# Kernel optimization log

Hardware: AMD Instinct MI355X
Metric: run time of the kernel (lower is better)

Reference implementation:

```python
import jax, jax.numpy as jnp
import numpy as np

N = 50000
E = 1600000
NFEAT = 256
NHID = 256
PAD_N = 60000


def setup_inputs() -> dict:
    key = jax.random.key(0)
    ks = jax.random.split(key, 8)
    x = jax.random.normal(ks[0], (N, NFEAT), dtype=jnp.float32)
    adj_rows = jax.random.randint(ks[1], (E,), 0, N)
    adj_cols = jax.random.randint(ks[2], (E,), 0, N)
    adj_vals = jax.random.uniform(ks[3], (E,), dtype=jnp.float32)
    pos_idx = jnp.arange(N)  # unique rows within padded output
    W1 = jax.random.normal(ks[4], (NFEAT, NHID), dtype=jnp.float32) * 0.05
    b1 = jax.random.normal(ks[5], (NHID,), dtype=jnp.float32) * 0.05
    W2 = jax.random.normal(ks[6], (NHID, NHID), dtype=jnp.float32) * 0.05
    b2 = jax.random.normal(ks[7], (NHID,), dtype=jnp.float32) * 0.05
    return {"x": x, "adj_rows": adj_rows, "adj_cols": adj_cols,
            "adj_vals": adj_vals, "pad_n": PAD_N, "pos_idx": pos_idx,
            "W1": W1, "b1": b1, "W2": W2, "b2": b2}


def _graph_conv(x, rows, cols, vals, W, b):
    # support = x @ W ; out = adj @ support + b  (adj in COO form)
    support = x @ W                                   # [N, H]
    msgs = vals[:, None] * support[cols]              # [E, H] gather + scale
    agg = jax.ops.segment_sum(msgs, rows, num_segments=x.shape[0])
    return agg + b


def reference(x, adj_rows, adj_cols, adj_vals, pad_n, pos_idx, W1, b1, W2, b2):
    h = jax.nn.relu(_graph_conv(x, adj_rows, adj_cols, adj_vals, W1, b1))
    # dropout: eval mode (training=False) -> identity
    h = jax.nn.relu(_graph_conv(h, adj_rows, adj_cols, adj_vals, W2, b2))
    out = jnp.zeros((pad_n, h.shape[1]), dtype=h.dtype)
    out = out.at[pos_idx].set(h)
    return out
```

## Files before the change

kernel.cpp:

```cpp
#include <hip/hip_runtime.h>
#include <hip/hip_bf16.h>

typedef __attribute__((ext_vector_type(8))) short short8;
typedef __attribute__((ext_vector_type(4))) float f32x4;
typedef __attribute__((ext_vector_type(2))) float f32x2;

#define BUK_SHIFT 7
#define BUK_ROWS 128
#define MAXBUK 512
#define ACAP 6144
#define CAP2 6144
#define CHUNK 6250
#define CHUNK_PAD 6272

static __device__ __forceinline__ unsigned short f2bf(float f) {
    unsigned u = __float_as_uint(f);
    u += 0x7fffu + ((u >> 16) & 1u);
    return (unsigned short)(u >> 16);
}
static __device__ __forceinline__ unsigned pk2bf(float a, float b) {
    return (unsigned)f2bf(a) | ((unsigned)f2bf(b) << 16);
}

__global__ void wtr_kernel(const float* __restrict__ W1, const float* __restrict__ W2,
                           unsigned short* __restrict__ W1t, unsigned short* __restrict__ W2t) {
    int k = blockIdx.x, n = threadIdx.x;
    const float* W = blockIdx.y ? W2 : W1;
    unsigned short* Wt = blockIdx.y ? W2t : W1t;
    Wt[n * 256 + k] = f2bf(W[k * 256 + n]);
}

__global__ __launch_bounds__(1024) void bin_scatter(const int* __restrict__ rows,
                                                    const int* __restrict__ cols,
                                                    const float* __restrict__ vals,
                                                    int* __restrict__ cursor,
                                                    unsigned int* __restrict__ cc,
                                                    unsigned char* __restrict__ rb,
                                                    int E, int nbuk) {
    __shared__ unsigned int scc[CHUNK_PAD];
    __shared__ unsigned char srb[CHUNK_PAD];
    __shared__ int lcnt[MAXBUK], lsc[MAXBUK], lcur[MAXBUK], gbase[MAXBUK];
    const int b = blockIdx.x, tid = threadIdx.x;
    const int s = b * CHUNK, e = s + CHUNK < E ? s + CHUNK : E;
    if (tid < MAXBUK) lcnt[tid] = 0;
    __syncthreads();
    for (int i = s + tid; i < e; i += 1024) atomicAdd(&lcnt[rows[i] >> BUK_SHIFT], 1);
    __syncthreads();
    if (tid < nbuk) gbase[tid] = atomicAdd(&cursor[tid], lcnt[tid]);
    if (tid < MAXBUK) lsc[tid] = lcnt[tid];
    __syncthreads();
    for (int off = 1; off < MAXBUK; off <<= 1) {
        int t = (tid < MAXBUK && tid >= off) ? lsc[tid - off] : 0;
        __syncthreads();
        if (tid < MAXBUK) lsc[tid] += t;
        __syncthreads();
    }
    if (tid < MAXBUK) lcur[tid] = lsc[tid] - lcnt[tid];
    __syncthreads();
    for (int i = s + tid; i < e; i += 1024) {
        int r = rows[i];
        int p = atomicAdd(&lcur[r >> BUK_SHIFT], 1);
        scc[p] = ((unsigned)cols[i] << 16) | (unsigned)f2bf(vals[i]);
        srb[p] = (unsigned char)(r & (BUK_ROWS - 1));
    }
    __syncthreads();
    const int wv = tid >> 6, ln = tid & 63;
    for (int bu = wv; bu < nbuk; bu += 16) {
        const int lo = lsc[bu] - lcnt[bu];
        const int n = lcnt[bu];
        const int gb = bu * ACAP + gbase[bu];
        for (int j = ln; j < n; j += 64) {
            cc[gb + j] = scc[lo + j];
            rb[gb + j] = srb[lo + j];
        }
    }
}

__global__ __launch_bounds__(1024) void bucket_pad(const unsigned int* __restrict__ cc,
                                                   const unsigned char* __restrict__ rb,
                                                   const int* __restrict__ cursor,
                                                   unsigned int* __restrict__ cc2,
                                                   int2* __restrict__ rp,
                                                   int nbuk, int N) {
    __shared__ int cnt[BUK_ROWS];
    __shared__ int psc[BUK_ROWS];
    __shared__ int cur[BUK_ROWS];
    const int b = blockIdx.x;
    const int tid = threadIdx.x;
    const int base = b * ACAP;
    int sz = cursor[b];
    if (sz > ACAP) sz = ACAP;
    if (tid < BUK_ROWS) cnt[tid] = 0;
    __syncthreads();
    for (int i = tid; i < sz; i += 1024) atomicAdd(&cnt[rb[base + i]], 1);
    __syncthreads();
    if (tid < BUK_ROWS) psc[tid] = (cnt[tid] + 7) & ~7;
    __syncthreads();
    for (int off = 1; off < BUK_ROWS; off <<= 1) {
        int t = (tid < BUK_ROWS && tid >= off) ? psc[tid - off] : 0;
        __syncthreads();
        if (tid < BUK_ROWS) psc[tid] += t;
        __syncthreads();
    }
    if (tid < BUK_ROWS) {
        int c = cnt[tid];
        int pc = (c + 7) & ~7;
        int excl = psc[tid] - pc;
        cur[tid] = excl;
        int st = b * CAP2 + excl;
        rp[b * BUK_ROWS + tid] = make_int2(st, st + pc);
        for (int z = c; z < pc; ++z) cc2[(size_t)st + z] = 0u;
    }
    __syncthreads();
    for (int i = tid; i < sz; i += 1024) {
        int p = atomicAdd(&cur[rb[base + i]], 1);
        cc2[(size_t)b * CAP2 + p] = cc[base + i];
    }
}

template <int AF32>
static __device__ __forceinline__ uint4 load_frag(const char* p) {
    if (AF32) {
        const float* f = (const float*)p;
        float4 f0 = *reinterpret_cast<const float4*>(f);
        float4 f1 = *reinterpret_cast<const float4*>(f + 4);
        uint4 u;
        u.x = pk2bf(f0.x, f0.y); u.y = pk2bf(f0.z, f0.w);
        u.z = pk2bf(f1.x, f1.y); u.w = pk2bf(f1.z, f1.w);
        return u;
    }
    return *reinterpret_cast<const uint4*>(p);
}

template <int AF32>
__global__ __launch_bounds__(256) void gemm_kernel(const void* __restrict__ Av,
                                                   const unsigned short* __restrict__ Bt,
                                                   unsigned char* __restrict__ S8, int M) {
    __shared__ unsigned char lds[2][8192];
    const int esz = AF32 ? 4 : 2;
    const int tid = threadIdx.x;
    const int lane = tid & 63;
    const int wave = tid >> 6;
    const int m0 = blockIdx.x * 64;
    const int l15 = lane & 15;
    const int q = lane >> 4;
    const int sw = (l15 & 7) << 4;

    const int st_r0 = tid >> 3;
    const int st_c = tid & 7;
    const int st_off0 = st_r0 * 128 + ((st_c ^ (st_r0 & 7)) << 4);
    const int st_r1 = st_r0 + 32;
    const int st_off1 = st_r1 * 128 + ((st_c ^ (st_r1 & 7)) << 4);
    int row0 = m0 + st_r0; row0 = row0 < M ? row0 : 0;
    int row1 = m0 + st_r1; row1 = row1 < M ? row1 : 0;
    const char* s0p = (const char*)Av + ((size_t)row0 * 256 + st_c * 8) * esz;
    const char* s1p = (const char*)Av + ((size_t)row1 * 256 + st_c * 8) * esz;

    const unsigned short* bb = Bt + (size_t)(wave * 64 + l15) * 256 + q * 8;

    f32x4 acc[4][4] = {};

    uint4 s0 = load_frag<AF32>(s0p);
    uint4 s1 = load_frag<AF32>(s1p);
    *reinterpret_cast<uint4*>(&lds[0][st_off0]) = s0;
    *reinterpret_cast<uint4*>(&lds[0][st_off1]) = s1;
    __syncthreads();

#pragma unroll
    for (int it = 0; it < 4; ++it) {
        const int buf = it & 1;
        if (it < 3) {
            s0 = load_frag<AF32>(s0p + (size_t)(it + 1) * 64 * esz);
            s1 = load_frag<AF32>(s1p + (size_t)(it + 1) * 64 * esz);
        }
        const int kk = it * 64;
#pragma unroll
        for (int ks = 0; ks < 2; ++ks) {
            short8 a[4], b[4];
#pragma unroll
            for (int mf = 0; mf < 4; ++mf) {
                int r = mf * 16 + l15;
                a[mf] = *reinterpret_cast<const short8*>(
                    &lds[buf][r * 128 + ((ks * 64 + q * 16) ^ sw)]);
            }
#pragma unroll
            for (int nf = 0; nf < 4; ++nf)
                b[nf] = *reinterpret_cast<const short8*>(bb + (size_t)nf * 16 * 256 + kk + ks * 32);
#pragma unroll
            for (int mf = 0; mf < 4; ++mf)
#pragma unroll
                for (int nf = 0; nf < 4; ++nf)
                    acc[mf][nf] = __builtin_amdgcn_mfma_f32_16x16x32_bf16(b[nf], a[mf], acc[mf][nf], 0, 0, 0);
        }
        if (it < 3) {
            *reinterpret_cast<uint4*>(&lds[buf ^ 1][st_off0]) = s0;
            *reinterpret_cast<uint4*>(&lds[buf ^ 1][st_off1]) = s1;
        }
        __syncthreads();
    }

    const int g4 = q * 4;
#pragma unroll
    for (int mf = 0; mf < 4; ++mf) {
        int m = m0 + mf * 16 + l15;
        if (m < M) {
#pragma unroll
            for (int nf = 0; nf < 4; ++nf) {
                int p = __builtin_amdgcn_cvt_pk_fp8_f32(acc[mf][nf][0], acc[mf][nf][1], 0, false);
                p = __builtin_amdgcn_cvt_pk_fp8_f32(acc[mf][nf][2], acc[mf][nf][3], p, true);
                *reinterpret_cast<int*>(S8 + ((size_t)wave * M + m) * 64 + nf * 16 + g4) = p;
            }
        }
    }
}

template <int LAYER2>
__global__ __launch_bounds__(256) void spmm_kernel(const unsigned char* __restrict__ S8,
                                                   const int2* __restrict__ rp,
                                                   const unsigned int* __restrict__ cc,
                                                   const float* __restrict__ bias,
                                                   unsigned short* __restrict__ out_bf,
                                                   float* __restrict__ out_f,
                                                   const int* __restrict__ pos_idx, int N) {
    const int slab = blockIdx.y;
    const int lane = threadIdx.x & 63;
    const int wid = threadIdx.x >> 6;
    const int q = lane >> 4;
    const int l = lane & 15;
    const int row = blockIdx.x * 16 + wid * 4 + q;
    const int2 r = rp[row];
    const unsigned lbyte = (unsigned)l * 4;
    const unsigned char* __restrict__ Sb = S8 + (size_t)slab * N * 64;
    f32x2 a01 = {0.f, 0.f}, a23 = {0.f, 0.f};
    int i = r.x;
    if (i < r.y) {
        uint4 c0 = *reinterpret_cast<const uint4*>(cc + i);
        uint4 c1 = *reinterpret_cast<const uint4*>(cc + i + 4);
        for (; i < r.y; i += 8) {
            uint4 n0 = *reinterpret_cast<const uint4*>(cc + i + 8);
            uint4 n1 = *reinterpret_cast<const uint4*>(cc + i + 12);
            unsigned cw[8] = {c0.x, c0.y, c0.z, c0.w, c1.x, c1.y, c1.z, c1.w};
            unsigned w[8];
#pragma unroll
            for (int e = 0; e < 8; ++e) {
                unsigned off = ((cw[e] >> 10) & 0xFFFFFFC0u) | lbyte;
                w[e] = *reinterpret_cast<const unsigned*>(Sb + off);
            }
#pragma unroll
            for (int e = 0; e < 8; ++e) {
                float v = __uint_as_float(cw[e] << 16);
                f32x2 vv = {v, v};
                a01 += vv * __builtin_amdgcn_cvt_pk_f32_fp8((int)w[e], false);
                a23 += vv * __builtin_amdgcn_cvt_pk_f32_fp8((int)w[e], true);
            }
            c0 = n0; c1 = n1;
        }
    }
    if (row >= N) return;
    const int f = slab * 64 + l * 4;
    float a0 = fmaxf(a01.x + bias[f + 0], 0.f);
    float a1 = fmaxf(a01.y + bias[f + 1], 0.f);
    float a2 = fmaxf(a23.x + bias[f + 2], 0.f);
    float a3 = fmaxf(a23.y + bias[f + 3], 0.f);
    if (LAYER2) {
        int orow = pos_idx[row];
        *reinterpret_cast<float4*>(out_f + (size_t)orow * 256 + f) = make_float4(a0, a1, a2, a3);
    } else {
        ushort4 o;
        o.x = f2bf(a0); o.y = f2bf(a1); o.z = f2bf(a2); o.w = f2bf(a3);
        *reinterpret_cast<ushort4*>(out_bf + (size_t)row * 256 + f) = o;
    }
}

extern "C" void kernel_launch(void* const* d_in, const int* in_sizes, int n_in,
                              void* d_out, int out_size, void* d_ws, size_t ws_size,
                              hipStream_t stream) {
    const float* x        = (const float*)d_in[0];
    const int* adj_rows   = (const int*)d_in[1];
    const int* adj_cols   = (const int*)d_in[2];
    const float* adj_vals = (const float*)d_in[3];
    const int* pos_idx    = (const int*)d_in[5];
    const float* W1       = (const float*)d_in[6];
    const float* b1       = (const float*)d_in[7];
    const float* W2       = (const float*)d_in[8];
    const float* b2       = (const float*)d_in[9];

    const int N = in_sizes[0] / 256;
    const int E = in_sizes[1];
    const int nbuk = (N + BUK_ROWS - 1) >> BUK_SHIFT;
    const int nblk = (E + CHUNK - 1) / CHUNK;
    const int nwork = nbuk * BUK_ROWS;

    char* ws = (char*)d_ws;
    size_t off = 0;
    auto alloc = [&](size_t bytes) {
        char* p = ws + off;
        off += (bytes + 255) & ~(size_t)255;
        return p;
    };
    unsigned short* xb   = (unsigned short*)alloc((size_t)N * 256 * 2);
    unsigned char*  sup8 = (unsigned char*)alloc((size_t)N * 256);
    unsigned short* w1t  = (unsigned short*)alloc(256 * 256 * 2);
    unsigned short* w2t  = (unsigned short*)alloc(256 * 256 * 2);
    int2* rp     = (int2*)alloc((size_t)nwork * 8);
    int* cursor  = (int*)alloc((size_t)nbuk * 4);
    unsigned int* cc  = (unsigned int*)alloc((size_t)nbuk * ACAP * 4);
    unsigned char* rb = (unsigned char*)alloc((size_t)nbuk * ACAP);
    unsigned int* cc2 = (unsigned int*)alloc((size_t)nbuk * CAP2 * 4);
    (void)ws_size; (void)n_in;

    hipMemsetAsync((float*)d_out + (size_t)N * 256, 0,
                   ((size_t)out_size - (size_t)N * 256) * 4, stream);
    hipMemsetAsync(cursor, 0, (size_t)nbuk * 4, stream);

    wtr_kernel<<<dim3(256, 2), 256, 0, stream>>>(W1, W2, w1t, w2t);

    bin_scatter<<<nblk, 1024, 0, stream>>>(adj_rows, adj_cols, adj_vals, cursor, cc, rb, E, nbuk);
    bucket_pad<<<nbuk, 1024, 0, stream>>>(cc, rb, cursor, cc2, rp, nbuk, N);

    const int ggrid = (N + 63) / 64;
    const dim3 sgrid(nwork / 16, 4);
    gemm_kernel<1><<<ggrid, 256, 0, stream>>>(x, w1t, sup8, N);
    spmm_kernel<0><<<sgrid, 256, 0, stream>>>(sup8, rp, cc2, b1, xb, nullptr, nullptr, N);
    gemm_kernel<0><<<ggrid, 256, 0, stream>>>(xb, w2t, sup8, N);
    spmm_kernel<1><<<sgrid, 256, 0, stream>>>(sup8, rp, cc2, b2, nullptr, (float*)d_out, pos_idx, N);
}
```

Baseline: 212.3 us.

## Merge prep kernels and run bucket padding alongside the first GEMM

Folds the weight transpose and the output tail zeroing into the edge binning kernel as extra blocks. It also merges the per-bucket padding/sort pass into the first-layer GEMM launch as additional blocks, since the two are independent. This removes several launches and one memset, and lets the sparse preprocessing overlap with dense compute. The padding blocks now run with 256 threads instead of 1024, so each of those blocks does more serial work.

```diff
diff --git a/kernel.cpp b/kernel.cpp
--- a/kernel.cpp
+++ b/kernel.cpp
@@ -12,6 +12,8 @@
 #define CAP2 6144
 #define CHUNK 6250
 #define CHUNK_PAD 6272
+#define NW_BLK 128
+#define NZ_BLK 40
 
 static __device__ __forceinline__ unsigned short f2bf(float f) {
     unsigned u = __float_as_uint(f);
@@ -22,25 +24,38 @@
     return (unsigned)f2bf(a) | ((unsigned)f2bf(b) << 16);
 }
 
-__global__ void wtr_kernel(const float* __restrict__ W1, const float* __restrict__ W2,
-                           unsigned short* __restrict__ W1t, unsigned short* __restrict__ W2t) {
-    int k = blockIdx.x, n = threadIdx.x;
-    const float* W = blockIdx.y ? W2 : W1;
-    unsigned short* Wt = blockIdx.y ? W2t : W1t;
-    Wt[n * 256 + k] = f2bf(W[k * 256 + n]);
-}
-
-__global__ __launch_bounds__(1024) void bin_scatter(const int* __restrict__ rows,
+__global__ __launch_bounds__(1024) void prep_kernel(const int* __restrict__ rows,
                                                     const int* __restrict__ cols,
                                                     const float* __restrict__ vals,
                                                     int* __restrict__ cursor,
                                                     unsigned int* __restrict__ cc,
                                                     unsigned char* __restrict__ rb,
-                                                    int E, int nbuk) {
+                                                    int E, int nbuk, int nblk,
+                                                    const float* __restrict__ W1,
+                                                    const float* __restrict__ W2,
+                                                    unsigned short* __restrict__ W1t,
+                                                    unsigned short* __restrict__ W2t,
+                                                    float* __restrict__ ztail, int nzf4) {
     __shared__ unsigned int scc[CHUNK_PAD];
     __shared__ unsigned char srb[CHUNK_PAD];
     __shared__ int lcnt[MAXBUK], lsc[MAXBUK], lcur[MAXBUK], gbase[MAXBUK];
     const int b = blockIdx.x, tid = threadIdx.x;
+    if (b >= nblk) {
+        if (b < nblk + NW_BLK) {
+            int idx = (b - nblk) * 1024 + tid;
+            int w = idx >> 16, rem = idx & 65535;
+            int k = rem >> 8, n = rem & 255;
+            const float* W = w ? W2 : W1;
+            unsigned short* Wt = w ? W2t : W1t;
+            Wt[n * 256 + k] = f2bf(W[k * 256 + n]);
+        } else {
+            float4* z4 = reinterpret_cast<float4*>(ztail);
+            int start = (b - nblk - NW_BLK) * 1024 + tid;
+            for (int i = start; i < nzf4; i += NZ_BLK * 1024)
+                z4[i] = make_float4(0.f, 0.f, 0.f, 0.f);
+        }
+        return;
+    }
     const int s = b * CHUNK, e = s + CHUNK < E ? s + CHUNK : E;
     if (tid < MAXBUK) lcnt[tid] = 0;
     __syncthreads();
@@ -73,48 +88,6 @@
             cc[gb + j] = scc[lo + j];
             rb[gb + j] = srb[lo + j];
         }
-    }
-}
-
-__global__ __launch_bounds__(1024) void bucket_pad(const unsigned int* __restrict__ cc,
-                                                   const unsigned char* __restrict__ rb,
-                                                   const int* __restrict__ cursor,
-                                                   unsigned int* __restrict__ cc2,
-                                                   int2* __restrict__ rp,
-                                                   int nbuk, int N) {
-    __shared__ int cnt[BUK_ROWS];
-    __shared__ int psc[BUK_ROWS];
-    __shared__ int cur[BUK_ROWS];
-    const int b = blockIdx.x;
-    const int tid = threadIdx.x;
-    const int base = b * ACAP;
-    int sz = cursor[b];
-    if (sz > ACAP) sz = ACAP;
-    if (tid < BUK_ROWS) cnt[tid] = 0;
-    __syncthreads();
-    for (int i = tid; i < sz; i += 1024) atomicAdd(&cnt[rb[base + i]], 1);
-    __syncthreads();
-    if (tid < BUK_ROWS) psc[tid] = (cnt[tid] + 7) & ~7;
-    __syncthreads();
-    for (int off = 1; off < BUK_ROWS; off <<= 1) {
-        int t = (tid < BUK_ROWS && tid >= off) ? psc[tid - off] : 0;
-        __syncthreads();
-        if (tid < BUK_ROWS) psc[tid] += t;
-        __syncthreads();
-    }
-    if (tid < BUK_ROWS) {
-        int c = cnt[tid];
-        int pc = (c + 7) & ~7;
-        int excl = psc[tid] - pc;
-        cur[tid] = excl;
-        int st = b * CAP2 + excl;
-        rp[b * BUK_ROWS + tid] = make_int2(st, st + pc);
-        for (int z = c; z < pc; ++z) cc2[(size_t)st + z] = 0u;
-    }
-    __syncthreads();
-    for (int i = tid; i < sz; i += 1024) {
-        int p = atomicAdd(&cur[rb[base + i]], 1);
-        cc2[(size_t)b * CAP2 + p] = cc[base + i];
     }
 }
 
@@ -133,15 +106,16 @@
 }
 
 template <int AF32>
-__global__ __launch_bounds__(256) void gemm_kernel(const void* __restrict__ Av,
-                                                   const unsigned short* __restrict__ Bt,
-                                                   unsigned char* __restrict__ S8, int M) {
-    __shared__ unsigned char lds[2][8192];
+static __device__ __forceinline__ void gemm_body(const void* __restrict__ Av,
+                                                 const unsigned short* __restrict__ Bt,
+                                                 unsigned char* __restrict__ S8, int M,
+                                                 int bx, unsigned char* lds_raw) {
+    unsigned char (*lds)[8192] = reinterpret_cast<unsigned char (*)[8192]>(lds_raw);
     const int esz = AF32 ? 4 : 2;
     const int tid = threadIdx.x;
     const int lane = tid & 63;
     const int wave = tid >> 6;
-    const int m0 = blockIdx.x * 64;
+    const int m0 = bx * 64;
     const int l15 = lane & 15;
     const int q = lane >> 4;
     const int sw = (l15 & 7) << 4;
@@ -212,6 +186,63 @@
             }
         }
     }
+}
+
+__global__ __launch_bounds__(256) void padgemm_kernel(const float* __restrict__ x,
+                                                      const unsigned short* __restrict__ W1t,
+                                                      unsigned char* __restrict__ S8, int M,
+                                                      int ggrid,
+                                                      const unsigned int* __restrict__ cc,
+                                                      const unsigned char* __restrict__ rb,
+                                                      const int* __restrict__ cursor,
+                                                      unsigned int* __restrict__ cc2,
+                                                      int2* __restrict__ rp, int nbuk) {
+    __shared__ unsigned char lds_raw[2 * 8192];
+    const int bx = blockIdx.x, tid = threadIdx.x;
+    if (bx < ggrid) {
+        gemm_body<1>(x, W1t, S8, M, bx, lds_raw);
+        return;
+    }
+    int* cnt = reinterpret_cast<int*>(lds_raw);
+    int* psc = cnt + BUK_ROWS;
+    int* cur = psc + BUK_ROWS;
+    const int b = bx - ggrid;
+    const int base = b * ACAP;
+    int sz = cursor[b];
+    if (sz > ACAP) sz = ACAP;
+    if (tid < BUK_ROWS) cnt[tid] = 0;
+    __syncthreads();
+    for (int i = tid; i < sz; i += 256) atomicAdd(&cnt[rb[base + i]], 1);
+    __syncthreads();
+    if (tid < BUK_ROWS) psc[tid] = (cnt[tid] + 7) & ~7;
+    __syncthreads();
+    for (int off = 1; off < BUK_ROWS; off <<= 1) {
+        int t = (tid < BUK_ROWS && tid >= off) ? psc[tid - off] : 0;
+        __syncthreads();
+        if (tid < BUK_ROWS) psc[tid] += t;
+        __syncthreads();
+    }
+    if (tid < BUK_ROWS) {
+        int c = cnt[tid];
+        int pc = (c + 7) & ~7;
+        int excl = psc[tid] - pc;
+        cur[tid] = excl;
+        int st = b * CAP2 + excl;
+        rp[b * BUK_ROWS + tid] = make_int2(st, st + pc);
+        for (int z = c; z < pc; ++z) cc2[(size_t)st + z] = 0u;
+    }
+    __syncthreads();
+    for (int i = tid; i < sz; i += 256) {
+        int p = atomicAdd(&cur[rb[base + i]], 1);
+        cc2[(size_t)b * CAP2 + p] = cc[base + i];
+    }
+}
+
+__global__ __launch_bounds__(256) void gemm_kernel(const unsigned short* __restrict__ A,
+                                                   const unsigned short* __restrict__ Bt,
+                                                   unsigned char* __restrict__ S8, int M) {
+    __shared__ unsigned char lds_raw[2 * 8192];
+    gemm_body<0>(A, Bt, S8, M, blockIdx.x, lds_raw);
 }
 
 template <int LAYER2>
@@ -309,19 +340,21 @@
     unsigned int* cc2 = (unsigned int*)alloc((size_t)nbuk * CAP2 * 4);
     (void)ws_size; (void)n_in;
 
-    hipMemsetAsync((float*)d_out + (size_t)N * 256, 0,
-                   ((size_t)out_size - (size_t)N * 256) * 4, stream);
     hipMemsetAsync(cursor, 0, (size_t)nbuk * 4, stream);
 
-    wtr_kernel<<<dim3(256, 2), 256, 0, stream>>>(W1, W2, w1t, w2t);
-
-    bin_scatter<<<nblk, 1024, 0, stream>>>(adj_rows, adj_cols, adj_vals, cursor, cc, rb, E, nbuk);
-    bucket_pad<<<nbuk, 1024, 0, stream>>>(cc, rb, cursor, cc2, rp, nbuk, N);
+    float* ztail = (float*)d_out + (size_t)N * 256;
+    const int nzf4 = (out_size - N * 256) / 4;
+
+    prep_kernel<<<nblk + NW_BLK + NZ_BLK, 1024, 0, stream>>>(
+        adj_rows, adj_cols, adj_vals, cursor, cc, rb, E, nbuk, nblk,
+        W1, W2, w1t, w2t, ztail, nzf4);
 
     const int ggrid = (N + 63) / 64;
     const dim3 sgrid(nwork / 16, 4);
-    gemm_kernel<1><<<ggrid, 256, 0, stream>>>(x, w1t, sup8, N);
+
+    padgemm_kernel<<<ggrid + nbuk, 256, 0, stream>>>(x, w1t, sup8, N, ggrid,
+                                                     cc, rb, cursor, cc2, rp, nbuk);
     spmm_kernel<0><<<sgrid, 256, 0, stream>>>(sup8, rp, cc2, b1, xb, nullptr, nullptr, N);
-    gemm_kernel<0><<<ggrid, 256, 0, stream>>>(xb, w2t, sup8, N);
+    gemm_kernel<<<ggrid, 256, 0, stream>>>(xb, w2t, sup8, N);
     spmm_kernel<1><<<sgrid, 256, 0, stream>>>(sup8, rp, cc2, b2, nullptr, (float*)d_out, pos_idx, N);
 }
```

Result: faster. 202.2 us (median of 2 runs) (-4.7%).
